# Kernel tuning notes

Hardware: AMD Instinct MI355X
Metric: run time of the kernel (lower is better)

## Reference

```python
import jax, jax.numpy as jnp
import numpy as np

B, T, H, W, C = 16, 24, 96, 96, 8
F = 16  # ConvLSTM filters
BN_EPS = 1e-3


def _conv(x, w):
    # x: [B,H,W,Cin], w: [kh,kw,Cin,Cout], SAME padding, stride 1
    return jax.lax.conv_general_dilated(
        x, w, window_strides=(1, 1), padding='SAME',
        dimension_numbers=('NHWC', 'HWIO', 'NHWC'))


def _hard_sigmoid(x):
    # Keras hard_sigmoid: clip(0.2*x + 0.5, 0, 1)
    return jnp.clip(0.2 * x + 0.5, 0.0, 1.0)


def setup_inputs() -> dict:
    key = jax.random.key(0)
    ks = jax.random.split(key, 8)
    inputs = jax.random.normal(ks[0], (B, T, H, W, C), dtype=jnp.float32)
    # ConvLSTM2D params: input kernel [3,3,C,4F] (gates i,f,c,o), recurrent kernel [3,3,F,4F], bias [4F]
    w_x = jax.random.normal(ks[1], (3, 3, C, 4 * F), dtype=jnp.float32) * 0.05
    w_h = jax.random.normal(ks[2], (3, 3, F, 4 * F), dtype=jnp.float32) * 0.05
    b = jnp.zeros((4 * F,), dtype=jnp.float32)
    # BatchNorm (inference mode, moving stats)
    gamma = jnp.ones((F,), dtype=jnp.float32) + 0.1 * jax.random.normal(ks[3], (F,), dtype=jnp.float32)
    beta = 0.1 * jax.random.normal(ks[4], (F,), dtype=jnp.float32)
    moving_mean = jnp.zeros((F,), dtype=jnp.float32)
    moving_var = jnp.ones((F,), dtype=jnp.float32)
    # Dense(1)
    dense_w = jax.random.normal(ks[5], (F, 1), dtype=jnp.float32) * 0.1
    dense_b = jnp.zeros((1,), dtype=jnp.float32)
    return {'inputs': inputs, 'w_x': w_x, 'w_h': w_h, 'b': b,
            'gamma': gamma, 'beta': beta,
            'moving_mean': moving_mean, 'moving_var': moving_var,
            'dense_w': dense_w, 'dense_b': dense_b}


def _convlstm(inputs, w_x, w_h, b):
    # inputs: [B,T,H,W,C] -> final hidden state [B,H,W,F]
    x_tbhwc = jnp.transpose(inputs, (1, 0, 2, 3, 4))  # time-major for scan

    def step(carry, x_t):
        h, c = carry
        z = _conv(x_t, w_x) + b + _conv(h, w_h)  # [B,H,W,4F]
        zi, zf, zc, zo = jnp.split(z, 4, axis=-1)
        i = _hard_sigmoid(zi)
        f = _hard_sigmoid(zf)
        c_new = f * c + i * jax.nn.relu(zc)  # cell activation overridden to relu
        o = _hard_sigmoid(zo)
        h_new = o * jax.nn.relu(c_new)
        return (h_new, c_new), None

    h0 = jnp.zeros((inputs.shape[0], inputs.shape[2], inputs.shape[3], F), dtype=inputs.dtype)
    (h_last, _), _ = jax.lax.scan(step, (h0, h0), x_tbhwc)
    return h_last


def reference(inputs, w_x, w_h, b, gamma, beta, moving_mean, moving_var, dense_w, dense_b):
    h = _convlstm(inputs, w_x, w_h, b)  # [B,H,W,F]
    # BatchNorm (inference): normalize with moving stats
    inv = gamma * jax.lax.rsqrt(moving_var + BN_EPS)
    x = h * inv + (beta - moving_mean * inv)
    # Dense(1) over channel dim
    out = jnp.einsum('bhwc,cd->bhwd', x, dense_w) + dense_b  # [B,H,W,1]
    return out
```

## Files before the change

### kernel.cpp

```cpp
#include <hip/hip_runtime.h>

#define NB 16
#define NT 24
#define NH 96
#define NW 96
#define NC 8
#define NF 16
#define NG 64
#define HW (NH*NW)
#define KPAD 224

typedef _Float16 f16x8 __attribute__((ext_vector_type(8)));
typedef float    f32x4 __attribute__((ext_vector_type(4)));

__global__ __launch_bounds__(256) void prep_weights(
    const float* __restrict__ wx, const float* __restrict__ wh,
    _Float16* __restrict__ wT)
{
    const int idx = blockIdx.x * 256 + threadIdx.x;
    if (idx >= NG * KPAD) return;
    const int n = idx / KPAD;
    const int k = idx % KPAD;
    float v = 0.f;
    if (k < 144)      v = wh[k * NG + n];
    else if (k < 216) v = wx[(k - 144) * NG + n];
    wT[n * KPAD + k] = (_Float16)v;
}

__global__ __launch_bounds__(256) void convlstm_step_mfma(
    const float* __restrict__ x,
    const _Float16* __restrict__ wT,
    const float* __restrict__ bias,
    const _Float16* __restrict__ h_in,
    _Float16* __restrict__ h_out,
    float* __restrict__ c,
    int t)
{
    __shared__ _Float16 hs[18 * 18 * NF];
    __shared__ _Float16 xs[18 * 18 * NC];
    __shared__ _Float16 ws[NG * KPAD];

    const int tid  = threadIdx.x;
    const int wave = tid >> 6;
    const int lane = tid & 63;
    const int g    = lane >> 4;
    const int cl   = lane & 15;

    const int b    = blockIdx.x / 36;
    const int tile = blockIdx.x % 36;
    const int ty0  = (tile / 6) * 16;
    const int tx0  = (tile % 6) * 16;

    {
        const f16x8* src = (const f16x8*)wT;
        f16x8*       dst = (f16x8*)ws;
        #pragma unroll
        for (int i = 0; i < (NG * KPAD / 8) / 256; ++i)
            dst[i * 256 + tid] = src[i * 256 + tid];
    }

    const _Float16* hb = h_in + (size_t)b * HW * NF;
    for (int i = tid; i < 324; i += 256) {
        const int gy = ty0 + (i / 18) - 1;
        const int gx = tx0 + (i % 18) - 1;
        f16x8 v0 = (f16x8)(_Float16)0.f, v1 = v0;
        if (gy >= 0 && gy < NH && gx >= 0 && gx < NW) {
            const f16x8* src = (const f16x8*)(hb + ((size_t)gy * NW + gx) * NF);
            v0 = src[0]; v1 = src[1];
        }
        *(f16x8*)&hs[i * NF]     = v0;
        *(f16x8*)&hs[i * NF + 8] = v1;
    }

    const float* xb = x + ((size_t)b * NT + t) * (size_t)HW * NC;
    for (int i = tid; i < 324; i += 256) {
        const int gy = ty0 + (i / 18) - 1;
        const int gx = tx0 + (i % 18) - 1;
        f16x8 v = (f16x8)(_Float16)0.f;
        if (gy >= 0 && gy < NH && gx >= 0 && gx < NW) {
            const float4* src = (const float4*)(xb + ((size_t)gy * NW + gx) * NC);
            float4 a0 = src[0], a1 = src[1];
            v[0] = (_Float16)a0.x; v[1] = (_Float16)a0.y;
            v[2] = (_Float16)a0.z; v[3] = (_Float16)a0.w;
            v[4] = (_Float16)a1.x; v[5] = (_Float16)a1.y;
            v[6] = (_Float16)a1.z; v[7] = (_Float16)a1.w;
        }
        *(f16x8*)&xs[i * NC] = v;
    }

    __syncthreads();

    f32x4 acc[4][4];
    #pragma unroll
    for (int nf = 0; nf < 4; ++nf) {
        const float bv = bias[nf * 16 + cl];
        #pragma unroll
        for (int mf = 0; mf < 4; ++mf) acc[mf][nf] = (f32x4)bv;
    }

    #pragma unroll
    for (int cc = 0; cc < 7; ++cc) {
        f16x8 bfr[4];
        #pragma unroll
        for (int nf = 0; nf < 4; ++nf)
            bfr[nf] = *(const f16x8*)&ws[(nf * 16 + cl) * KPAD + cc * 32 + g * 8];

        const int khat = cc * 32 + g * 8;
        f16x8 afr[4];
        #pragma unroll
        for (int mf = 0; mf < 4; ++mf) {
            const int ty = (wave << 2) + mf;
            f16x8 a;
            if (khat < 144) {
                const int tap = khat >> 4;
                const int ci0 = khat & 15;
                a = *(const f16x8*)&hs[((ty + tap / 3) * 18 + cl + tap % 3) * NF + ci0];
            } else if (khat < 216) {
                const int tap = (khat - 144) >> 3;
                a = *(const f16x8*)&xs[((ty + tap / 3) * 18 + cl + tap % 3) * NC];
            } else {
                a = (f16x8)(_Float16)0.f;
            }
            afr[mf] = a;
        }

        #pragma unroll
        for (int mf = 0; mf < 4; ++mf)
            #pragma unroll
            for (int nf = 0; nf < 4; ++nf)
                acc[mf][nf] = __builtin_amdgcn_mfma_f32_16x16x32_f16(
                    afr[mf], bfr[nf], acc[mf][nf], 0, 0, 0);
    }

    #pragma unroll
    for (int mf = 0; mf < 4; ++mf) {
        const int gy = ty0 + (wave << 2) + mf;
        #pragma unroll
        for (int r = 0; r < 4; ++r) {
            const int gx = tx0 + (g << 2) + r;
            const size_t pix = (size_t)b * HW + (size_t)gy * NW + gx;
            const float zi = acc[mf][0][r];
            const float zf = acc[mf][1][r];
            const float zc = acc[mf][2][r];
            const float zo = acc[mf][3][r];
            const float ig = fminf(fmaxf(0.2f * zi + 0.5f, 0.f), 1.f);
            const float fg = fminf(fmaxf(0.2f * zf + 0.5f, 0.f), 1.f);
            const float og = fminf(fmaxf(0.2f * zo + 0.5f, 0.f), 1.f);
            const float cold = c[pix * NF + cl];
            const float cn = fg * cold + ig * fmaxf(zc, 0.f);
            c[pix * NF + cl] = cn;
            h_out[pix * NF + cl] = (_Float16)(og * fmaxf(cn, 0.f));
        }
    }
}

__global__ __launch_bounds__(256) void bn_dense(
    const _Float16* __restrict__ h,
    const float* __restrict__ gamma,
    const float* __restrict__ beta,
    const float* __restrict__ mean,
    const float* __restrict__ var,
    const float* __restrict__ dw,
    const float* __restrict__ db,
    float* __restrict__ out)
{
    const int p = blockIdx.x * 256 + threadIdx.x;
    if (p >= NB * HW) return;

    const f16x8* hp = (const f16x8*)(h + (size_t)p * NF);
    f16x8 h0 = hp[0], h1 = hp[1];
    float s = db[0];
    float dot = 0.f;
    #pragma unroll
    for (int k = 0; k < NF; ++k) {
        const float inv = gamma[k] / sqrtf(var[k] + 1e-3f);
        const float hv = (k < 8) ? (float)h0[k] : (float)h1[k - 8];
        s   += (beta[k] - mean[k] * inv) * dw[k];
        dot += hv * inv * dw[k];
    }
    out[p] = s + dot;
}

extern "C" void kernel_launch(void* const* d_in, const int* in_sizes, int n_in,
                              void* d_out, int out_size, void* d_ws, size_t ws_size,
                              hipStream_t stream) {
    const float* x     = (const float*)d_in[0];
    const float* wx    = (const float*)d_in[1];
    const float* wh    = (const float*)d_in[2];
    const float* bias  = (const float*)d_in[3];
    const float* gamma = (const float*)d_in[4];
    const float* beta  = (const float*)d_in[5];
    const float* mean  = (const float*)d_in[6];
    const float* var   = (const float*)d_in[7];
    const float* dw    = (const float*)d_in[8];
    const float* db    = (const float*)d_in[9];
    float* out = (float*)d_out;

    const size_t nh = (size_t)NB * HW * NF;
    _Float16* h0 = (_Float16*)d_ws;
    _Float16* h1 = h0 + nh;
    float*    cc = (float*)(h1 + nh);
    _Float16* wT = (_Float16*)(cc + nh);

    hipMemsetAsync(h0, 0, nh * sizeof(_Float16), stream);
    hipMemsetAsync(cc, 0, nh * sizeof(float), stream);

    prep_weights<<<(NG * KPAD + 255) / 256, 256, 0, stream>>>(wx, wh, wT);

    const int blocks = NB * 36;
    for (int t = 0; t < NT; ++t) {
        const _Float16* hin  = (t & 1) ? h1 : h0;
        _Float16*       hout = (t & 1) ? h0 : h1;
        convlstm_step_mfma<<<blocks, 256, 0, stream>>>(x, wT, bias, hin, hout, cc, t);
    }
    bn_dense<<<NB * HW / 256, 256, 0, stream>>>(h0, gamma, beta, mean, var, dw, db, out);
}
```

Measured before the change: 502.7 us.

## Keep weight fragments in registers and pad hidden-state LDS to cut bank conflicts

Removes the 28KB weight staging into shared memory and instead loads each lane's B fragments for all seven K-chunks directly from global memory into registers. It pads the hidden-state LDS rows to a 24-element stride to reduce bank conflicts, and precomputes per-chunk A-fragment base pointers with a zero-pad buffer so the inner loop has no branches. Launch bounds now request two blocks per SIMD. The goal is lower LDS usage, higher occupancy, and less per-block weight copying, at the cost of more VGPRs per lane and uncoalesced global weight reads.

```diff
diff --git a/kernel.cpp b/kernel.cpp
--- a/kernel.cpp
+++ b/kernel.cpp
@@ -9,6 +9,7 @@
 #define NG 64
 #define HW (NH*NW)
 #define KPAD 224
+#define HSTR 24
 
 typedef _Float16 f16x8 __attribute__((ext_vector_type(8)));
 typedef float    f32x4 __attribute__((ext_vector_type(4)));
@@ -27,7 +28,7 @@
     wT[n * KPAD + k] = (_Float16)v;
 }
 
-__global__ __launch_bounds__(256) void convlstm_step_mfma(
+__global__ __launch_bounds__(256, 2) void convlstm_step_mfma(
     const float* __restrict__ x,
     const _Float16* __restrict__ wT,
     const float* __restrict__ bias,
@@ -36,9 +37,9 @@
     float* __restrict__ c,
     int t)
 {
-    __shared__ _Float16 hs[18 * 18 * NF];
+    __shared__ _Float16 hs[18 * 18 * HSTR];
     __shared__ _Float16 xs[18 * 18 * NC];
-    __shared__ _Float16 ws[NG * KPAD];
+    __shared__ __align__(16) _Float16 zpad[8];
 
     const int tid  = threadIdx.x;
     const int wave = tid >> 6;
@@ -51,13 +52,14 @@
     const int ty0  = (tile / 6) * 16;
     const int tx0  = (tile % 6) * 16;
 
-    {
-        const f16x8* src = (const f16x8*)wT;
-        f16x8*       dst = (f16x8*)ws;
-        #pragma unroll
-        for (int i = 0; i < (NG * KPAD / 8) / 256; ++i)
-            dst[i * 256 + tid] = src[i * 256 + tid];
-    }
+    f16x8 bfr[7][4];
+    #pragma unroll
+    for (int cc = 0; cc < 7; ++cc)
+        #pragma unroll
+        for (int nf = 0; nf < 4; ++nf)
+            bfr[cc][nf] = *(const f16x8*)&wT[(nf * 16 + cl) * KPAD + cc * 32 + g * 8];
+
+    if (tid == 0) *(f16x8*)zpad = (f16x8)(_Float16)0.f;
 
     const _Float16* hb = h_in + (size_t)b * HW * NF;
     for (int i = tid; i < 324; i += 256) {
@@ -68,8 +70,8 @@
             const f16x8* src = (const f16x8*)(hb + ((size_t)gy * NW + gx) * NF);
             v0 = src[0]; v1 = src[1];
         }
-        *(f16x8*)&hs[i * NF]     = v0;
-        *(f16x8*)&hs[i * NF + 8] = v1;
+        *(f16x8*)&hs[i * HSTR]     = v0;
+        *(f16x8*)&hs[i * HSTR + 8] = v1;
     }
 
     const float* xb = x + ((size_t)b * NT + t) * (size_t)HW * NC;
@@ -88,48 +90,48 @@
         *(f16x8*)&xs[i * NC] = v;
     }
 
+    const _Float16* abase[7];
+    int astr[7];
+    #pragma unroll
+    for (int cc = 0; cc < 7; ++cc) {
+        const int khat = cc * 32 + g * 8;
+        if (khat < 144) {
+            const int tap = khat >> 4, ci0 = khat & 15;
+            abase[cc] = &hs[(((wave * 4) + tap / 3) * 18 + cl + tap % 3) * HSTR + ci0];
+            astr[cc]  = 18 * HSTR;
+        } else if (khat < 216) {
+            const int tap = (khat - 144) >> 3;
+            abase[cc] = &xs[(((wave * 4) + tap / 3) * 18 + cl + tap % 3) * NC];
+            astr[cc]  = 18 * NC;
+        } else {
+            abase[cc] = zpad;
+            astr[cc]  = 0;
+        }
+    }
+
+    float bv[4];
+    #pragma unroll
+    for (int nf = 0; nf < 4; ++nf) bv[nf] = bias[nf * 16 + cl];
+    f32x4 acc[4][4];
+    #pragma unroll
+    for (int mf = 0; mf < 4; ++mf)
+        #pragma unroll
+        for (int nf = 0; nf < 4; ++nf) acc[mf][nf] = (f32x4)bv[nf];
+
     __syncthreads();
 
-    f32x4 acc[4][4];
-    #pragma unroll
-    for (int nf = 0; nf < 4; ++nf) {
-        const float bv = bias[nf * 16 + cl];
-        #pragma unroll
-        for (int mf = 0; mf < 4; ++mf) acc[mf][nf] = (f32x4)bv;
-    }
-
     #pragma unroll
     for (int cc = 0; cc < 7; ++cc) {
-        f16x8 bfr[4];
-        #pragma unroll
-        for (int nf = 0; nf < 4; ++nf)
-            bfr[nf] = *(const f16x8*)&ws[(nf * 16 + cl) * KPAD + cc * 32 + g * 8];
-
-        const int khat = cc * 32 + g * 8;
         f16x8 afr[4];
         #pragma unroll
-        for (int mf = 0; mf < 4; ++mf) {
-            const int ty = (wave << 2) + mf;
-            f16x8 a;
-            if (khat < 144) {
-                const int tap = khat >> 4;
-                const int ci0 = khat & 15;
-                a = *(const f16x8*)&hs[((ty + tap / 3) * 18 + cl + tap % 3) * NF + ci0];
-            } else if (khat < 216) {
-                const int tap = (khat - 144) >> 3;
-                a = *(const f16x8*)&xs[((ty + tap / 3) * 18 + cl + tap % 3) * NC];
-            } else {
-                a = (f16x8)(_Float16)0.f;
-            }
-            afr[mf] = a;
-        }
-
+        for (int mf = 0; mf < 4; ++mf)
+            afr[mf] = *(const f16x8*)(abase[cc] + mf * astr[cc]);
         #pragma unroll
         for (int mf = 0; mf < 4; ++mf)
             #pragma unroll
             for (int nf = 0; nf < 4; ++nf)
                 acc[mf][nf] = __builtin_amdgcn_mfma_f32_16x16x32_f16(
-                    afr[mf], bfr[nf], acc[mf][nf], 0, 0, 0);
+                    afr[mf], bfr[cc][nf], acc[mf][nf], 0, 0, 0);
     }
 
     #pragma unroll
```

Result: slower. 561.6 us (+11.7%).
